# Optimization experiments

Hardware: AMD Instinct MI355X
Metric: run time of the kernel (lower is better)

## Reference

```python
import jax, jax.numpy as jnp
import numpy as np

N_NODES = 6890
N_ANGLES = 8
K_CHEB = 15
N_DESC = 544
HIDDEN = 64
N_CLASS = 6890
M = N_ANGLES * N_NODES  # 55120, size of anisotropic Laplacian
DEG = 16
NNZ = M * DEG
BN_EPS = 1e-5


def setup_inputs() -> dict:
    key = jax.random.key(0)
    ks = jax.random.split(key, 16)
    x = jax.random.normal(ks[0], (N_NODES, N_DESC), dtype=jnp.float32)
    # sparse anisotropic Laplacian (M x M), ~DEG nnz per row
    rows = jnp.repeat(jnp.arange(M, dtype=jnp.int32), DEG)
    cols = jax.random.randint(ks[1], (NNZ,), 0, M, dtype=jnp.int32)
    vals = jax.random.normal(ks[2], (NNZ,), dtype=jnp.float32) * 0.1
    # conv1: (K, n_angles*n_desc, 64); conv2..6 stacked: (5, K, n_angles*64, 64)
    def xavier(k, shape, fan_in, fan_out):
        lim = np.sqrt(6.0 / (fan_in + fan_out))
        return jax.random.uniform(k, shape, jnp.float32, -lim, lim)
    W1 = xavier(ks[3], (K_CHEB, N_ANGLES * N_DESC, HIDDEN), N_ANGLES * N_DESC, HIDDEN)
    Wc = xavier(ks[4], (5, K_CHEB, N_ANGLES * HIDDEN, HIDDEN), N_ANGLES * HIDDEN, HIDDEN)
    conv_b = jnp.zeros((6, HIDDEN), jnp.float32)
    bn_gamma = jnp.ones((6, HIDDEN), jnp.float32)
    bn_beta = jnp.zeros((6, HIDDEN), jnp.float32)
    fc2_w = xavier(ks[5], (HIDDEN, 256), HIDDEN, 256)
    fc2_b = jnp.zeros((256,), jnp.float32)
    fc3_w = xavier(ks[6], (256, N_CLASS), 256, N_CLASS)
    fc3_b = jnp.zeros((N_CLASS,), jnp.float32)
    return {"x": x, "rows": rows, "cols": cols, "vals": vals,
            "W1": W1, "Wc": Wc, "conv_b": conv_b,
            "bn_gamma": bn_gamma, "bn_beta": bn_beta,
            "fc2_w": fc2_w, "fc2_b": fc2_b, "fc3_w": fc3_w, "fc3_b": fc3_b}


def _spmm(rows, cols, vals, T):
    # (M x M sparse) @ (M x C) via gather + segment-sum
    return jax.ops.segment_sum(vals[:, None] * T[cols], rows, num_segments=M)


def _acs_conv(x, rows, cols, vals, W, b):
    # x: (N, C). Chebyshev recurrence on the (A*N, C) angle-stacked signal.
    N, C = x.shape
    A = N_ANGLES

    def proj(T, Wk):
        # (A*N, C) -> (N, A*C) @ (A*C, out)
        return T.reshape(A, N, C).transpose(1, 0, 2).reshape(N, A * C) @ Wk

    T0 = jnp.tile(x, (A, 1))
    out = proj(T0, W[0])
    T1 = _spmm(rows, cols, vals, T0)
    out = out + proj(T1, W[1])
    for k in range(2, K_CHEB):
        T2 = 2.0 * _spmm(rows, cols, vals, T1) - T0
        out = out + proj(T2, W[k])
        T0, T1 = T1, T2
    return out + b


def _bn_relu(x, gamma, beta):
    # BatchNorm1d (training-mode batch stats, biased variance) + ReLU
    mean = jnp.mean(x, axis=0)
    var = jnp.var(x, axis=0)
    return jax.nn.relu((x - mean) * jax.lax.rsqrt(var + BN_EPS) * gamma + beta)


def reference(x, rows, cols, vals, W1, Wc, conv_b, bn_gamma, bn_beta,
              fc2_w, fc2_b, fc3_w, fc3_b):
    h = _bn_relu(_acs_conv(x, rows, cols, vals, W1, conv_b[0]), bn_gamma[0], bn_beta[0])
    for i in range(5):
        h = _bn_relu(_acs_conv(h, rows, cols, vals, Wc[i], conv_b[i + 1]),
                     bn_gamma[i + 1], bn_beta[i + 1])
    h = jax.nn.relu(h @ fc2_w + fc2_b)
    # dropout is identity at inference
    return h @ fc3_w + fc3_b
```

## Files before the change

### kernel.cpp

```cpp
#include <hip/hip_runtime.h>
#include <cstdint>
#include <cstddef>

#define NN 6890
#define NA 8
#define KC 15
#define ND 544
#define MR (NA * NN)
#define DEG 16
#define NNZ (MR * DEG)
#define BN_EPS 1e-5f
#define NRG 108
#define PB (NA * NRG)
#define NB64  1723

typedef unsigned int u32;
typedef _Float16 f16;
typedef __attribute__((ext_vector_type(8))) _Float16 f16x8;
typedef __attribute__((ext_vector_type(4))) _Float16 f16x4;
typedef __attribute__((ext_vector_type(4))) float f32x4;

union U4H8 { uint4 q; f16 h[8]; f16x8 v; };

struct Slabs4 { const uint4* s[4]; };

__device__ __forceinline__ u32 packh(float a, float b) {
    union { f16 h[2]; u32 u; } c;
    c.h[0] = (f16)a; c.h[1] = (f16)b; return c.u;
}
__device__ __forceinline__ uint4 pack8h(const float* t) {
    uint4 m;
    m.x = packh(t[0], t[1]); m.y = packh(t[2], t[3]);
    m.z = packh(t[4], t[5]); m.w = packh(t[6], t[7]);
    return m;
}
__device__ __forceinline__ void acc8h(float* s, float v, uint4 g) {
    U4H8 c; c.q = g;
    #pragma unroll
    for (int i = 0; i < 8; ++i) s[i] += v * (float)c.h[i];
}

__global__ __launch_bounds__(256)
void prep_cv_kernel(const int* __restrict__ cols, const float* __restrict__ vals,
                    uint4* __restrict__ cvq)
{
    const int q = blockIdx.x * 256 + threadIdx.x;
    if (q >= NNZ / 4) return;
    const int4   c = ((const int4*)cols)[q];
    const float4 v = ((const float4*)vals)[q];
    uint4 o;
    o.x = ((u32)c.x & 0xffffu) | ((u32)c.y << 16);
    o.y = ((u32)c.z & 0xffffu) | ((u32)c.w << 16);
    o.z = packh(v.x, v.y);
    o.w = packh(v.z, v.w);
    cvq[q] = o;
}

template<int CC, bool BN>
__device__ __forceinline__
void tile_body(int bid, const float* __restrict__ X, int C_in, int c0,
               uint4* __restrict__ slab0, const float* __restrict__ bnp)
{
    constexpr int LPR = CC / 8;
    constexpr int RPB = 256 / LPR;
    const int tid = threadIdx.x;
    const int j = tid % LPR, rloc = tid / LPR;
    const int r = bid * RPB + rloc;
    if (r >= MR) return;
    const int n = r % NN;
    const float* xp = X + (size_t)n * C_in + c0 + 8 * j;
    const float4 t0 = *(const float4*)xp;
    const float4 t1 = *(const float4*)(xp + 4);
    float t[8] = { t0.x, t0.y, t0.z, t0.w, t1.x, t1.y, t1.z, t1.w };
    if (BN) {
        const int ch = c0 + 8 * j;
        #pragma unroll
        for (int i = 0; i < 8; ++i) {
            const float v = t[i] * bnp[ch + i] + bnp[64 + ch + i];
            t[i] = v > 0.f ? v : 0.f;
        }
    }
    slab0[(size_t)r * LPR + j] = pack8h(t);
}

template<int CC>
__global__ __launch_bounds__(256)
void tile_any_kernel(const float* __restrict__ X, int C_in, int c0,
                     uint4* __restrict__ slab0)
{
    tile_body<CC, false>(blockIdx.x, X, C_in, c0, slab0, nullptr);
}

__global__ __launch_bounds__(256)
void tile64_bn_kernel(const float* __restrict__ X, uint4* __restrict__ slab0,
                      const float* __restrict__ bnp)
{
    tile_body<64, true>(blockIdx.x, X, 64, 0, slab0, bnp);
}

template<int CC, bool CHEB>
__device__ __forceinline__
void spmm_body(int bid, const uint4* __restrict__ sp, const uint4* __restrict__ sc,
               uint4* __restrict__ sw, const uint4* __restrict__ cvq, uint4* cvl)
{
    constexpr int LPR = CC / 8;
    constexpr int RPB = 256 / LPR;
    const int tid = threadIdx.x;
    const int j = tid % LPR, rloc = tid / LPR;
    const int r0 = bid * RPB;
    const int nrow = (MR - r0) < RPB ? (MR - r0) : RPB;
    for (int e = tid; e < nrow * 4; e += 256)
        cvl[e] = cvq[(size_t)r0 * 4 + e];
    __syncthreads();
    const int r = r0 + rloc;
    if (r >= MR) return;

    int c[16]; float v[16];
    #pragma unroll
    for (int q = 0; q < 4; ++q) {
        const uint4 cq = cvl[rloc * 4 + q];
        c[4 * q + 0] = cq.x & 0xffffu; c[4 * q + 1] = cq.x >> 16;
        c[4 * q + 2] = cq.y & 0xffffu; c[4 * q + 3] = cq.y >> 16;
        union { u32 u; f16 h[2]; } z, w_;
        z.u = cq.z; w_.u = cq.w;
        v[4 * q + 0] = (float)z.h[0]; v[4 * q + 1] = (float)z.h[1];
        v[4 * q + 2] = (float)w_.h[0]; v[4 * q + 3] = (float)w_.h[1];
    }
    float s[8] = {0.f, 0.f, 0.f, 0.f, 0.f, 0.f, 0.f, 0.f};
    #pragma unroll
    for (int d = 0; d < DEG; ++d)
        acc8h(s, v[d], sp[(size_t)c[d] * LPR + j]);
    float t[8];
    if (CHEB) {
        U4H8 p; p.q = sc[(size_t)r * LPR + j];
        #pragma unroll
        for (int i = 0; i < 8; ++i) t[i] = 2.f * s[i] - (float)p.h[i];
    } else {
        #pragma unroll
        for (int i = 0; i < 8; ++i) t[i] = s[i];
    }
    sw[(size_t)r * LPR + j] = pack8h(t);
}

template<int CC, bool CHEB>
__global__ __launch_bounds__(256)
void spmm_any_kernel(const uint4* __restrict__ sp, const uint4* __restrict__ sc,
                     uint4* __restrict__ sw, const uint4* __restrict__ cvq)
{
    __shared__ uint4 cvl[256];
    spmm_body<CC, CHEB>(blockIdx.x, sp, sc, sw, cvq, cvl);
}

template<bool FIRSTP>
__device__ __forceinline__
void proj_ld(f32x4 (&acc)[4], const float* __restrict__ part, int a, int rows0,
             int l, int w)
{
    const int hi16 = l >> 4;
    #pragma unroll
    for (int nt = 0; nt < 4; ++nt)
        #pragma unroll
        for (int rr = 0; rr < 4; ++rr) {
            const int orow = rows0 + w * 16 + hi16 * 4 + rr;
            float vv = 0.f;
            if (!FIRSTP && orow < NN)
                vv = part[((size_t)a * NN + orow) * 64 + nt * 16 + (l & 15)];
            acc[nt][rr] = vv;
        }
}

__device__ __forceinline__
void proj_st(const f32x4 (&acc)[4], float* __restrict__ part, int a, int rows0,
             int l, int w)
{
    const int hi16 = l >> 4;
    #pragma unroll
    for (int nt = 0; nt < 4; ++nt)
        #pragma unroll
        for (int rr = 0; rr < 4; ++rr) {
            const int orow = rows0 + w * 16 + hi16 * 4 + rr;
            if (orow < NN)
                part[((size_t)a * NN + orow) * 64 + nt * 16 + (l & 15)] = acc[nt][rr];
        }
}

template<int SCC, int NPROJ>
__device__ __forceinline__
void proj_accum(int a, int rows0, int l, int w, Slabs4 sl,
                const float* __restrict__ W, int C_in, int c0, int kbase,
                u32* WH, u32* WL, f32x4 (&acc)[4], bool presync)
{
    constexpr int LPRF   = SCC / 8;
    constexpr int SLICES = SCC >= 64 ? SCC / 64 : 1;
    constexpr int SCH    = SCC >= 64 ? 64 : SCC;
    constexpr int CCH    = SCH / 32;
    const int tid = threadIdx.x;
    const int hi16 = l >> 4;
    const int arow = rows0 + w * 16 + (l & 15);
    const int arc  = arow < NN ? arow : NN - 1;
    const size_t abase = (size_t)(a * NN + arc) * LPRF;

    #pragma unroll
    for (int p = 0; p < NPROJ; ++p) {
        const uint4* slab = sl.s[p];
        #pragma unroll
        for (int s = 0; s < SLICES; ++s) {
            const float* Wk = W + ((size_t)(kbase + p) * NA * C_in
                                   + (size_t)a * C_in + c0 + s * 64) * 64;
            if (p | s) __syncthreads();
            else if (presync) __syncthreads();
            for (int e = tid; e < CCH * 1024; e += 256) {
                const int i2 = e & 3;
                const int ll = (e >> 2) & 63;
                const int nt = (e >> 8) & 3;
                const int h  = e >> 10;
                const int cc  = h * 32 + (ll >> 4) * 8 + 2 * i2;
                const int col = nt * 16 + (ll & 15);
                const float w0 = Wk[(size_t)cc * 64 + col];
                const float w1 = Wk[(size_t)(cc + 1) * 64 + col];
                const f16 h0 = (f16)w0, h1 = (f16)w1;
                union { f16 h[2]; u32 u; } ph, pl;
                ph.h[0] = h0; ph.h[1] = h1;
                pl.h[0] = (f16)(w0 - (float)h0); pl.h[1] = (f16)(w1 - (float)h1);
                WH[e] = ph.u; WL[e] = pl.u;
            }
            __syncthreads();
            #pragma unroll
            for (int h = 0; h < CCH; ++h) {
                U4H8 af; af.q = slab[abase + s * 8 + h * 4 + hi16];
                #pragma unroll
                for (int nt = 0; nt < 4; ++nt) {
                    const int be = ((h * 4 + nt) * 64 + l) * 4;
                    U4H8 bh, bl;
                    bh.q = *(const uint4*)&WH[be];
                    bl.q = *(const uint4*)&WL[be];
                    acc[nt] = __builtin_amdgcn_mfma_f32_16x16x32_f16(af.v, bh.v, acc[nt], 0, 0, 0);
                    acc[nt] = __builtin_amdgcn_mfma_f32_16x16x32_f16(af.v, bl.v, acc[nt], 0, 0, 0);
                }
            }
        }
    }
}

template<int CC, bool FIRSTP>
__global__ __launch_bounds__(256)
void step_any_proj_kernel(const uint4* __restrict__ sp, const uint4* __restrict__ sc,
                          uint4* __restrict__ sw, const uint4* __restrict__ cvq,
                          const float* __restrict__ W, float* __restrict__ part,
                          int C_in, int c0, int kbase, int NB)
{
    __shared__ uint4 cvl[256];
    __shared__ u32 WH[2048];
    __shared__ u32 WL[2048];
    const int bid = blockIdx.x;
    if (bid < NB) { spmm_body<CC, true>(bid, sp, sc, sw, cvq, cvl); return; }
    const int pb = bid - NB;
    const int l = threadIdx.x & 63, w = threadIdx.x >> 6;
    const int a = pb / NRG, rows0 = (pb % NRG) * 64;
    f32x4 acc[4];
    proj_ld<FIRSTP>(acc, part, a, rows0, l, w);
    Slabs4 s2; s2.s[0] = sc; s2.s[1] = sp;
    proj_accum<CC, 2>(a, rows0, l, w, s2, W, C_in, c0, kbase, WH, WL, acc, false);
    proj_st(acc, part, a, rows0, l, w);
}

template<int CC>
__global__ __launch_bounds__(256)
void proj_any_final_kernel(const uint4* __restrict__ sl, const float* __restrict__ W,
                           float* __restrict__ part, int C_in, int c0, int kproj)
{
    __shared__ u32 WH[2048];
    __shared__ u32 WL[2048];
    const int pb = blockIdx.x;
    const int l = threadIdx.x & 63, w = threadIdx.x >> 6;
    const int a = pb / NRG, rows0 = (pb % NRG) * 64;
    f32x4 acc[4];
    proj_ld<false>(acc, part, a, rows0, l, w);
    Slabs4 s1; s1.s[0] = sl;
    proj_accum<CC, 1>(a, rows0, l, w, s1, W, C_in, c0, kproj, WH, WL, acc, false);
    proj_st(acc, part, a, rows0, l, w);
}

template<bool FIRSTP>
__global__ __launch_bounds__(256)
void step64_proj4_kernel(const uint4* __restrict__ sp, const uint4* __restrict__ sc,
                         uint4* __restrict__ sw, Slabs4 prj,
                         const uint4* __restrict__ cvq, const float* __restrict__ W,
                         float* __restrict__ part, int kbase)
{
    __shared__ uint4 cvl[256];
    __shared__ u32 WH[2048];
    __shared__ u32 WL[2048];
    const int bid = blockIdx.x;
    if (bid < NB64) { spmm_body<64, true>(bid, sp, sc, sw, cvq, cvl); return; }
    const int pb = bid - NB64;
    const int l = threadIdx.x & 63, w = threadIdx.x >> 6;
    const int a = pb / NRG, rows0 = (pb % NRG) * 64;
    f32x4 acc[4];
    proj_ld<FIRSTP>(acc, part, a, rows0, l, w);
    proj_accum<64, 4>(a, rows0, l, w, prj, W, 64, 0, kbase, WH, WL, acc, false);
    proj_st(acc, part, a, rows0, l, w);
}

__global__ __launch_bounds__(256)
void proj64_final_kernel(Slabs4 prj, const float* __restrict__ W,
                         float* __restrict__ part, int kbase)
{
    __shared__ u32 WH[2048];
    __shared__ u32 WL[2048];
    const int pb = blockIdx.x;
    const int l = threadIdx.x & 63, w = threadIdx.x >> 6;
    const int a = pb / NRG, rows0 = (pb % NRG) * 64;
    f32x4 acc[4];
    proj_ld<false>(acc, part, a, rows0, l, w);
    proj_accum<64, 3>(a, rows0, l, w, prj, W, 64, 0, kbase, WH, WL, acc, false);
    proj_st(acc, part, a, rows0, l, w);
}

__global__ void bn_reduce_kernel(const float* __restrict__ part, float* __restrict__ acc)
{
    const int e = blockIdx.x * blockDim.x + threadIdx.x;
    if (e >= NN * 64) return;
    float s = 0.f;
    #pragma unroll
    for (int a = 0; a < NA; ++a) s += part[(size_t)a * NN * 64 + e];
    acc[e] = s;
}

__global__ __launch_bounds__(256)
void bn_stats_kernel(const float* __restrict__ acc, const float* __restrict__ gamma,
                     const float* __restrict__ beta, float* __restrict__ bnp)
{
    const int h = blockIdx.x;
    float s = 0.f, sq = 0.f;
    for (int n = threadIdx.x; n < NN; n += 256) {
        const float v = acc[(size_t)n * 64 + h];
        s += v; sq += v * v;
    }
    __shared__ float ls[256], lq[256];
    ls[threadIdx.x] = s; lq[threadIdx.x] = sq;
    __syncthreads();
    for (int st = 128; st > 0; st >>= 1) {
        if (threadIdx.x < st) { ls[threadIdx.x] += ls[threadIdx.x + st]; lq[threadIdx.x] += lq[threadIdx.x + st]; }
        __syncthreads();
    }
    if (threadIdx.x == 0) {
        const float mean = ls[0] / (float)NN;
        const float var  = lq[0] / (float)NN - mean * mean;
        const float sc   = gamma[h] / sqrtf(var + BN_EPS);
        bnp[h]      = sc;
        bnp[64 + h] = beta[h] - mean * sc;
    }
}

__global__ void bn_apply_kernel(const float* __restrict__ acc, const float* __restrict__ bnp,
                                float* __restrict__ H)
{
    const int e = blockIdx.x * blockDim.x + threadIdx.x;
    if (e >= NN * 64) return;
    const int h = e & 63;
    const float v = acc[e] * bnp[h] + bnp[64 + h];
    H[e] = v > 0.f ? v : 0.f;
}

__global__ __launch_bounds__(256)
void fc2_kernel(const float* __restrict__ A, const float* __restrict__ B,
                const float* __restrict__ bias,
                f16* __restrict__ Oh, f16* __restrict__ Ol)
{
    constexpr int Kk = 64, Nn = 256;
    __shared__ float As[16][132];
    __shared__ float Bs[16][132];
    const int tx = threadIdx.x & 15, ty = threadIdx.x >> 4;
    const int m0 = blockIdx.y * 128, n0 = blockIdx.x * 128;
    const bool full = (m0 + 128 <= NN);
    float acc[8][8] = {};
    for (int k0 = 0; k0 < Kk; k0 += 16) {
        if (full) {
            #pragma unroll
            for (int e = threadIdx.x; e < 512; e += 256) {
                const int i = e >> 2, q = e & 3;
                const float4 a4 = *(const float4*)&A[(size_t)(m0 + i) * Kk + k0 + 4 * q];
                As[4 * q + 0][i] = a4.x; As[4 * q + 1][i] = a4.y;
                As[4 * q + 2][i] = a4.z; As[4 * q + 3][i] = a4.w;
            }
        } else {
            for (int e = threadIdx.x; e < 128 * 16; e += 256) {
                const int i = e >> 4, kk = e & 15;
                const int row = m0 + i;
                As[kk][i] = (row < NN) ? A[(size_t)row * Kk + k0 + kk] : 0.f;
            }
        }
        #pragma unroll
        for (int e = threadIdx.x; e < 512; e += 256) {
            const int kk = e >> 5, q = e & 31;
            *(float4*)&Bs[kk][4 * q] = *(const float4*)&B[(size_t)(k0 + kk) * Nn + n0 + 4 * q];
        }
        __syncthreads();
        #pragma unroll
        for (int kk = 0; kk < 16; ++kk) {
            float av[8], bv[8];
            *(float4*)&av[0] = *(const float4*)&As[kk][ty * 4];
            *(float4*)&av[4] = *(const float4*)&As[kk][64 + ty * 4];
            *(float4*)&bv[0] = *(const float4*)&Bs[kk][tx * 4];
            *(float4*)&bv[4] = *(const float4*)&Bs[kk][64 + tx * 4];
            #pragma unroll
            for (int i = 0; i < 8; ++i)
                #pragma unroll
                for (int jj = 0; jj < 8; ++jj)
                    acc[i][jj] += av[i] * bv[jj];
        }
        __syncthreads();
    }
    #pragma unroll
    for (int i = 0; i < 8; ++i) {
        const int row = m0 + (i < 4 ? ty * 4 + i : 64 + ty * 4 + (i - 4));
        if (row >= NN) continue;
        #pragma unroll
        for (int g = 0; g < 2; ++g) {
            const int colg = n0 + (g ? 64 : 0) + tx * 4;
            f16x4 vh, vl;
            #pragma unroll
            for (int jj = 0; jj < 4; ++jj) {
                float v = acc[i][g * 4 + jj] + bias[colg + jj];
                v = fmaxf(v, 0.f);
                const f16 h = (f16)v;
                vh[jj] = h; vl[jj] = (f16)(v - (float)h);
            }
            const size_t ob = ((size_t)(colg >> 3) * NN + row) * 8 + (colg & 7);
            *(f16x4*)&Oh[ob] = vh;
            *(f16x4*)&Ol[ob] = vl;
        }
    }
}

__global__ __launch_bounds__(256)
void w3_split_kernel(const float* __restrict__ W, f16* __restrict__ Wh, f16* __restrict__ Wl)
{
    __shared__ float t[64][65];
    const int tid = threadIdx.x;
    const int n0 = blockIdx.x * 64, k0 = blockIdx.y * 64;
    for (int e = tid; e < 64 * 64; e += 256) {
        const int kk = e >> 6, nn = e & 63;
        const int gn = n0 + nn;
        t[kk][nn] = (gn < NN) ? W[(size_t)(k0 + kk) * NN + gn] : 0.f;
    }
    __syncthreads();
    for (int e = tid; e < 64 * 8; e += 256) {
        const int nn = e >> 3, c8 = e & 7;
        const int gn = n0 + nn;
        if (gn >= NN) continue;
        const size_t ob = ((size_t)((k0 >> 3) + c8) * NN + gn) * 8;
        f16 vh[8], vl[8];
        #pragma unroll
        for (int i = 0; i < 8; ++i) {
            const float w = t[c8 * 8 + i][nn];
            const f16 h = (f16)w;
            vh[i] = h; vl[i] = (f16)(w - (float)h);
        }
        *(uint4*)&Wh[ob] = *(const uint4*)vh;
        *(uint4*)&Wl[ob] = *(const uint4*)vl;
    }
}

__global__ __launch_bounds__(256)
void fc3_mfma_kernel(const f16* __restrict__ Ah, const f16* __restrict__ Al,
                     const f16* __restrict__ Bh, const f16* __restrict__ Bl,
                     const float* __restrict__ bias, float* __restrict__ C)
{
    const int o = blockIdx.x;
    const int xcd = o & 7, jj0 = o >> 3;
    const int wg = (xcd < 4 ? xcd * 365 : 4 * 365 + (xcd - 4) * 364) + jj0;
    const int band = wg / 486, inb = wg % 486;
    const int mt = inb / 9, nt = band * 9 + inb % 9;
    const int m0 = mt * 128, n0 = nt * 128;

    const int tid = threadIdx.x, l = tid & 63, w = tid >> 6;
    const int wm = w >> 1, wn = w & 1, hi16 = l >> 4;

    size_t aoff[4], boff[4];
    #pragma unroll
    for (int mf = 0; mf < 4; ++mf) {
        int row = m0 + wm * 64 + mf * 16 + (l & 15);
        if (row > NN - 1) row = NN - 1;
        aoff[mf] = (size_t)row * 8;
    }
    #pragma unroll
    for (int nf = 0; nf < 4; ++nf) {
        int col = n0 + wn * 64 + nf * 16 + (l & 15);
        if (col > NN - 1) col = NN - 1;
        boff[nf] = (size_t)col * 8;
    }

    f32x4 acc[4][4];
    #pragma unroll
    for (int mf = 0; mf < 4; ++mf)
        #pragma unroll
        for (int nf = 0; nf < 4; ++nf)
            acc[mf][nf] = (f32x4){0.f, 0.f, 0.f, 0.f};

    for (int k0 = 0; k0 < 256; k0 += 32) {
        const size_t cb = (size_t)((k0 >> 3) + hi16) * NN * 8;
        f16x8 ah[4], al[4], bh[4], bl[4];
        #pragma unroll
        for (int mf = 0; mf < 4; ++mf) {
            ah[mf] = *(const f16x8*)(Ah + cb + aoff[mf]);
            al[mf] = *(const f16x8*)(Al + cb + aoff[mf]);
        }
        #pragma unroll
        for (int nf = 0; nf < 4; ++nf) {
            bh[nf] = *(const f16x8*)(Bh + cb + boff[nf]);
            bl[nf] = *(const f16x8*)(Bl + cb + boff[nf]);
        }
        #pragma unroll
        for (int mf = 0; mf < 4; ++mf)
            #pragma unroll
            for (int nf = 0; nf < 4; ++nf) {
                acc[mf][nf] = __builtin_amdgcn_mfma_f32_16x16x32_f16(ah[mf], bh[nf], acc[mf][nf], 0, 0, 0);
                acc[mf][nf] = __builtin_amdgcn_mfma_f32_16x16x32_f16(ah[mf], bl[nf], acc[mf][nf], 0, 0, 0);
                acc[mf][nf] = __builtin_amdgcn_mfma_f32_16x16x32_f16(al[mf], bh[nf], acc[mf][nf], 0, 0, 0);
            }
    }

    #pragma unroll
    for (int mf = 0; mf < 4; ++mf) {
        #pragma unroll
        for (int nf = 0; nf < 4; ++nf) {
            const int col = n0 + wn * 64 + nf * 16 + (l & 15);
            if (col >= NN) continue;
            const float bv = bias[col];
            #pragma unroll
            for (int rr = 0; rr < 4; ++rr) {
                const int row = m0 + wm * 64 + mf * 16 + hi16 * 4 + rr;
                if (row < NN)
                    C[(size_t)row * NN + col] = acc[mf][nf][rr] + bv;
            }
        }
    }
}

template<int CC>
static void run_phase(bool first, const float* X, int c0, const uint4* cvq,
                      const float* W, uint4* ring, float* part, hipStream_t stream)
{
    constexpr int RPB = 256 / (CC / 8);
    const int NB = (MR + RPB - 1) / RPB;
    const size_t SLOT = (size_t)MR * (CC / 8);
    auto sl = [&](int k) { return ring + (size_t)(k % 3) * SLOT; };

    tile_any_kernel<CC><<<NB, 256, 0, stream>>>(X, ND, c0, sl(0));
    spmm_any_kernel<CC, false><<<NB, 256, 0, stream>>>(sl(0), sl(0), sl(1), cvq);
    for (int k = 2; k < KC; ++k) {
        if (k & 1) {
            spmm_any_kernel<CC, true><<<NB, 256, 0, stream>>>(sl(k - 1), sl(k - 2), sl(k), cvq);
        } else if (first && k == 2) {
            step_any_proj_kernel<CC, true ><<<NB + PB, 256, 0, stream>>>(
                sl(k - 1), sl(k - 2), sl(k), cvq, W, part, ND, c0, k - 2, NB);
        } else {
            step_any_proj_kernel<CC, false><<<NB + PB, 256, 0, stream>>>(
                sl(k - 1), sl(k - 2), sl(k), cvq, W, part, ND, c0, k - 2, NB);
        }
    }
    proj_any_final_kernel<CC><<<PB, 256, 0, stream>>>(sl(KC - 1), W, part, ND, c0, KC - 1);
}

extern "C" void kernel_launch(void* const* d_in, const int* in_sizes, int n_in,
                              void* d_out, int out_size, void* d_ws, size_t ws_size,
                              hipStream_t stream)
{
    (void)in_sizes; (void)n_in; (void)out_size; (void)ws_size;
    const float* x     = (const float*)d_in[0];
    const int*   cols  = (const int*)  d_in[2];
    const float* vals  = (const float*)d_in[3];
    const float* W1    = (const float*)d_in[4];
    const float* Wc    = (const float*)d_in[5];
    const float* gamma = (const float*)d_in[7];
    const float* beta  = (const float*)d_in[8];
    const float* fc2w  = (const float*)d_in[9];
    const float* fc2b  = (const float*)d_in[10];
    const float* fc3w  = (const float*)d_in[11];
    const float* fc3b  = (const float*)d_in[12];

    const size_t MT = (size_t)MR * 64;

    uint4* ring512 = (uint4*)d_out;
    uint4* ringT   = ring512 + 3 * (size_t)MR * 64;

    char* base = (char*)d_ws;
    size_t off = 0;
    uint4* cvq  = (uint4*)(base + off); off += (size_t)(NNZ / 4) * 16;
    uint4* ring5 = (uint4*)(base + off); off += 5 * (size_t)MR * 8 * 16;
    float* part = (float*)(base + off); off += MT * 4;
    float* acc  = (float*)(base + off); off += (size_t)NN * 64 * 4;
    float* H    = (float*)(base + off); off += (size_t)NN * 64 * 4;
    f16* f2h    = (f16*)(base + off);   off += (size_t)NN * 256 * 2;
    f16* f2l    = (f16*)(base + off);   off += (size_t)NN * 256 * 2;
    f16* W3h    = (f16*)(base + off);   off += (size_t)NN * 256 * 2;
    f16* W3l    = (f16*)(base + off);   off += (size_t)NN * 256 * 2;
    float* bnp  = (float*)(base + off);
    const size_t SL64 = (size_t)MR * 8;
    auto sl5 = [&](int k) { return ring5 + (size_t)(k % 5) * SL64; };

    prep_cv_kernel<<<(NNZ / 4 + 255) / 256, 256, 0, stream>>>(cols, vals, cvq);
    w3_split_kernel<<<dim3(108, 4), 256, 0, stream>>>(fc3w, W3h, W3l);

    {
        run_phase<512>(true,  x, 0,   cvq, W1, ring512, part, stream);
        run_phase<32 >(false, x, 512, cvq, W1, ringT,   part, stream);
        bn_reduce_kernel<<<(NN * 64 + 255) / 256, 256, 0, stream>>>(part, acc);
        bn_stats_kernel<<<64, 256, 0, stream>>>(acc, gamma, beta, bnp);
    }

    for (int li = 1; li < 6; ++li) {
        const float* W = Wc + (size_t)(li - 1) * KC * (NA * 64) * 64;
        tile64_bn_kernel<<<NB64, 256, 0, stream>>>(acc, sl5(0), bnp);
        spmm_any_kernel<64, false><<<NB64, 256, 0, stream>>>(sl5(0), sl5(0), sl5(1), cvq);
        for (int k = 2; k < KC; ++k) {
            if (k == 4 || k == 8 || k == 12) {
                Slabs4 prj;
                prj.s[0] = sl5(k - 4); prj.s[1] = sl5(k - 3);
                prj.s[2] = sl5(k - 2); prj.s[3] = sl5(k - 1);
                if (k == 4)
                    step64_proj4_kernel<true ><<<NB64 + PB, 256, 0, stream>>>(
                        sl5(k - 1), sl5(k - 2), sl5(k), prj, cvq, W, part, k - 4);
                else
                    step64_proj4_kernel<false><<<NB64 + PB, 256, 0, stream>>>(
                        sl5(k - 1), sl5(k - 2), sl5(k), prj, cvq, W, part, k - 4);
            } else {
                spmm_any_kernel<64, true><<<NB64, 256, 0, stream>>>(sl5(k - 1), sl5(k - 2), sl5(k), cvq);
            }
        }
        Slabs4 prjf;
        prjf.s[0] = sl5(12); prjf.s[1] = sl5(13); prjf.s[2] = sl5(14); prjf.s[3] = sl5(14);
        proj64_final_kernel<<<PB, 256, 0, stream>>>(prjf, W, part, 12);
        bn_reduce_kernel<<<(NN * 64 + 255) / 256, 256, 0, stream>>>(part, acc);
        bn_stats_kernel<<<64, 256, 0, stream>>>(acc, gamma + li * 64, beta + li * 64, bnp);
    }

    bn_apply_kernel<<<(NN * 64 + 255) / 256, 256, 0, stream>>>(acc, bnp, H);
    fc2_kernel<<<dim3(2, 54), 256, 0, stream>>>(H, fc2w, fc2b, f2h, f2l);
    fc3_mfma_kernel<<<2916, 256, 0, stream>>>(f2h, f2l, W3h, W3l, fc3b, (float*)d_out);
}
```

Baseline: 4.075 ms.

## Split first-layer 512-channel phase into two 256 phases; fuse BN apply into fc2

Result: no change. 4.038 ms (-0.9%).

```diff
diff --git a/kernel.cpp b/kernel.cpp
--- a/kernel.cpp
+++ b/kernel.cpp
@@ -353,19 +353,9 @@
     }
 }
 
-__global__ void bn_apply_kernel(const float* __restrict__ acc, const float* __restrict__ bnp,
-                                float* __restrict__ H)
-{
-    const int e = blockIdx.x * blockDim.x + threadIdx.x;
-    if (e >= NN * 64) return;
-    const int h = e & 63;
-    const float v = acc[e] * bnp[h] + bnp[64 + h];
-    H[e] = v > 0.f ? v : 0.f;
-}
-
-__global__ __launch_bounds__(256)
-void fc2_kernel(const float* __restrict__ A, const float* __restrict__ B,
-                const float* __restrict__ bias,
+__global__ __launch_bounds__(256)
+void fc2_kernel(const float* __restrict__ Acc, const float* __restrict__ bnp,
+                const float* __restrict__ B, const float* __restrict__ bias,
                 f16* __restrict__ Oh, f16* __restrict__ Ol)
 {
     constexpr int Kk = 64, Nn = 256;
@@ -380,15 +370,25 @@
             #pragma unroll
             for (int e = threadIdx.x; e < 512; e += 256) {
                 const int i = e >> 2, q = e & 3;
-                const float4 a4 = *(const float4*)&A[(size_t)(m0 + i) * Kk + k0 + 4 * q];
-                As[4 * q + 0][i] = a4.x; As[4 * q + 1][i] = a4.y;
-                As[4 * q + 2][i] = a4.z; As[4 * q + 3][i] = a4.w;
+                const float4 a4 = *(const float4*)&Acc[(size_t)(m0 + i) * Kk + k0 + 4 * q];
+                #pragma unroll
+                for (int cpt = 0; cpt < 4; ++cpt) {
+                    const int ch = k0 + 4 * q + cpt;
+                    const float raw = (&a4.x)[cpt] * bnp[ch] + bnp[64 + ch];
+                    As[4 * q + cpt][i] = raw > 0.f ? raw : 0.f;
+                }
             }
         } else {
             for (int e = threadIdx.x; e < 128 * 16; e += 256) {
                 const int i = e >> 4, kk = e & 15;
                 const int row = m0 + i;
-                As[kk][i] = (row < NN) ? A[(size_t)row * Kk + k0 + kk] : 0.f;
+                float vv = 0.f;
+                if (row < NN) {
+                    const int ch = k0 + kk;
+                    vv = Acc[(size_t)row * Kk + ch] * bnp[ch] + bnp[64 + ch];
+                    vv = vv > 0.f ? vv : 0.f;
+                }
+                As[kk][i] = vv;
             }
         }
         #pragma unroll
@@ -568,7 +568,7 @@
                               void* d_out, int out_size, void* d_ws, size_t ws_size,
                               hipStream_t stream)
 {
-    (void)in_sizes; (void)n_in; (void)out_size; (void)ws_size;
+    (void)in_sizes; (void)n_in; (void)out_size;
     const float* x     = (const float*)d_in[0];
     const int*   cols  = (const int*)  d_in[2];
     const float* vals  = (const float*)d_in[3];
@@ -582,22 +582,33 @@
     const float* fc3b  = (const float*)d_in[12];
 
     const size_t MT = (size_t)MR * 64;
-
-    uint4* ring512 = (uint4*)d_out;
-    uint4* ringT   = ring512 + 3 * (size_t)MR * 64;
+    const size_t REGION = 3 * (size_t)MR * 512;
+
+    const size_t FIXED = (size_t)(NNZ / 4) * 16
+                       + MT * 4
+                       + (size_t)NN * 64 * 4
+                       + (size_t)NN * 256 * 2 * 4
+                       + 1024;
+    const bool bigws = ws_size >= FIXED + REGION + (1 << 20);
 
     char* base = (char*)d_ws;
     size_t off = 0;
     uint4* cvq  = (uint4*)(base + off); off += (size_t)(NNZ / 4) * 16;
-    uint4* ring5 = (uint4*)(base + off); off += 5 * (size_t)MR * 8 * 16;
+    uint4* region;
+    if (bigws) { region = (uint4*)(base + off); off += REGION; }
+    else       { region = nullptr; off += 5 * (size_t)MR * 8 * 16; }
     float* part = (float*)(base + off); off += MT * 4;
     float* acc  = (float*)(base + off); off += (size_t)NN * 64 * 4;
-    float* H    = (float*)(base + off); off += (size_t)NN * 64 * 4;
     f16* f2h    = (f16*)(base + off);   off += (size_t)NN * 256 * 2;
     f16* f2l    = (f16*)(base + off);   off += (size_t)NN * 256 * 2;
     f16* W3h    = (f16*)(base + off);   off += (size_t)NN * 256 * 2;
     f16* W3l    = (f16*)(base + off);   off += (size_t)NN * 256 * 2;
     float* bnp  = (float*)(base + off);
+
+    uint4* ring256 = bigws ? region : (uint4*)d_out;
+    uint4* ringT   = bigws ? region : (uint4*)d_out + 3 * (size_t)MR * 32;
+    uint4* ring5   = bigws ? region : (uint4*)((char*)d_ws + (size_t)(NNZ / 4) * 16);
+
     const size_t SL64 = (size_t)MR * 8;
     auto sl5 = [&](int k) { return ring5 + (size_t)(k % 5) * SL64; };
 
@@ -605,7 +616,8 @@
     w3_split_kernel<<<dim3(108, 4), 256, 0, stream>>>(fc3w, W3h, W3l);
 
     {
-        run_phase<512>(true,  x, 0,   cvq, W1, ring512, part, stream);
+        run_phase<256>(true,  x, 0,   cvq, W1, ring256, part, stream);
+        run_phase<256>(false, x, 256, cvq, W1, ring256, part, stream);
         run_phase<32 >(false, x, 512, cvq, W1, ringT,   part, stream);
         bn_reduce_kernel<<<(NN * 64 + 255) / 256, 256, 0, stream>>>(part, acc);
         bn_stats_kernel<<<64, 256, 0, stream>>>(acc, gamma, beta, bnp);
@@ -637,7 +649,6 @@
         bn_stats_kernel<<<64, 256, 0, stream>>>(acc, gamma + li * 64, beta + li * 64, bnp);
     }
 
-    bn_apply_kernel<<<(NN * 64 + 255) / 256, 256, 0, stream>>>(acc, bnp, H);
-    fc2_kernel<<<dim3(2, 54), 256, 0, stream>>>(H, fc2w, fc2b, f2h, f2l);
+    fc2_kernel<<<dim3(2, 54), 256, 0, stream>>>(acc, bnp, fc2w, fc2b, f2h, f2l);
     fc3_mfma_kernel<<<2916, 256, 0, stream>>>(f2h, f2l, W3h, W3l, fc3b, (float*)d_out);
 }
```
